# Kernel optimization log

Hardware: AMD Instinct MI355X
Metric: run time of the kernel (lower is better)

Reference implementation:

```python
import jax, jax.numpy as jnp
import numpy as np

B, C_IN, H, W = 4, 256, 56, 56
REL, OUT, SP, K, PAD = 16, 256, 8, 7, 3
WS = OUT // SP            # 32 attention-weight channels
K2 = K * K                # 49 window taps
EPS = 1e-5


def _unfold(x, k, pad):
    # reflect-pad (SAN pad_mode=1 -> *_refpad kernels) then gather kxk window taps
    # x: [B,C,H,W] -> [B,C,k*k,H,W], tap order row-major (matches torch Unfold)
    xp = jnp.pad(x, ((0, 0), (0, 0), (pad, pad), (pad, pad)), mode='reflect')
    h, w = x.shape[2], x.shape[3]
    return jnp.stack([xp[:, :, i:i + h, j:j + w]
                      for i in range(k) for j in range(k)], axis=2)


def _conv1x1(x, w, b):
    return jnp.einsum('bchw,oc->bohw', x, w) + b[None, :, None, None]


def _bn(x, g, b, m, v):
    # eval-mode BatchNorm2d over channel axis 1, broadcast over trailing dims
    shape = (1, -1) + (1,) * (x.ndim - 2)
    scale = g.reshape(shape) * jax.lax.rsqrt(v.reshape(shape) + EPS)
    return (x - m.reshape(shape)) * scale + b.reshape(shape)


def _forward(x, w1, b1, w2, b2, w3, b3,
             bn1_g, bn1_b, bn1_m, bn1_v, cw1_w,
             bn2_g, bn2_b, bn2_m, bn2_v, cw2_w, cw2_b, pos2_w):
    x1 = _conv1x1(x, w1, b1)          # [B,REL,H,W]  (query)
    x2 = _conv1x1(x, w2, b2)          # [B,REL,H,W]  (key)
    x3 = _conv1x1(x, w3, b3)          # [B,OUT,H,W]  (value)

    # Subtraction2: q_i - k_j for each of K2 window taps -> [B,REL,K2,H,W]
    diff = x1[:, :, None, :, :] - _unfold(x2, K, PAAD) if False else x1[:, :, None, :, :] - _unfold(x2, K, PAD)

    # conv_w: BN -> ReLU -> 1x1 (no bias) -> BN -> ReLU -> 1x1 (bias)
    h = jax.nn.relu(_bn(diff, bn1_g, bn1_b, bn1_m, bn1_v))
    h = jnp.einsum('bckhw,oc->bokhw', h, cw1_w)
    h = jax.nn.relu(_bn(h, bn2_g, bn2_b, bn2_m, bn2_v))
    h = jnp.einsum('bckhw,oc->bokhw', h, cw2_w) + cw2_b[None, :, None, None, None]
    w = jax.nn.softmax(h, axis=2)     # softmax over K2 taps -> [B,WS,K2,H,W]

    # Aggregation: out[b,c,p] = sum_k unfold(x3)[b,c,k,p] * w[b, c//SP, k, p]
    unf3 = _unfold(x3, K, PAD).reshape(B, WS, SP, K2, H, W)
    agg = jnp.einsum('bgskhw,bgkhw->bgshw', unf3, w).reshape(B, OUT, H, W)

    # use_position2: interleave aggregated values with w, grouped 1x1 conv
    xv = agg.reshape(B, SP, WS, H, W).transpose(0, 2, 1, 3, 4)   # [B,WS,SP,H,W]
    xc = jnp.concatenate([xv, w], axis=2)                        # [B,WS,SP+K2,H,W]
    out = jnp.einsum('bgihw,goi->bgohw', xc, pos2_w).reshape(B, OUT, H, W)
    return out


def setup_inputs() -> dict:
    key = jax.random.key(0)
    ks = jax.random.split(key, 20)
    n = lambda k, s, sc=1.0: jax.random.normal(k, s, dtype=jnp.float32) * sc
    u = lambda k, s: jax.random.uniform(k, s, dtype=jnp.float32, minval=0.5, maxval=1.5)
    return {
        'x': n(ks[0], (B, C_IN, H, W)),
        'w1': n(ks[1], (REL, C_IN), 0.05), 'b1': n(ks[2], (REL,), 0.05),
        'w2': n(ks[3], (REL, C_IN), 0.05), 'b2': n(ks[4], (REL,), 0.05),
        'w3': n(ks[5], (OUT, C_IN), 0.05), 'b3': n(ks[6], (OUT,), 0.05),
        'bn1_g': u(ks[7], (REL,)), 'bn1_b': n(ks[8], (REL,), 0.1),
        'bn1_m': n(ks[9], (REL,), 0.1), 'bn1_v': u(ks[10], (REL,)),
        'cw1_w': n(ks[11], (REL, REL), 0.2),
        'bn2_g': u(ks[12], (REL,)), 'bn2_b': n(ks[13], (REL,), 0.1),
        'bn2_m': n(ks[14], (REL,), 0.1), 'bn2_v': u(ks[15], (REL,)),
        'cw2_w': n(ks[16], (WS, REL), 0.2), 'cw2_b': n(ks[17], (WS,), 0.05),
        'pos2_w': n(ks[18], (WS, SP, SP + K2), 0.1),
    }


def reference(x, w1, b1, w2, b2, w3, b3,
              bn1_g, bn1_b, bn1_m, bn1_v, cw1_w,
              bn2_g, bn2_b, bn2_m, bn2_v, cw2_w, cw2_b, pos2_w):
    return _forward(x, w1, b1, w2, b2, w3, b3,
                    bn1_g, bn1_b, bn1_m, bn1_v, cw1_w,
                    bn2_g, bn2_b, bn2_m, bn2_v, cw2_w, cw2_b, pos2_w)
```

## Files before the change

kernel.cpp:

```cpp
#include <hip/hip_runtime.h>

#define HW 56
#define NPIX 3136
#define CIN 256
#define OUTC 256

typedef unsigned short ushort_t;
typedef unsigned int uint_t;
typedef __attribute__((ext_vector_type(8))) short bf16x8;
typedef __attribute__((ext_vector_type(4))) float f32x4;
typedef __attribute__((ext_vector_type(2))) __fp16 half2v;
typedef __attribute__((ext_vector_type(4))) _Float16 f16x4;

__device__ __forceinline__ ushort_t f2b(float f){
  uint_t u = __float_as_uint(f);
  u += 0x7fffu + ((u>>16)&1u);
  return (ushort_t)(u>>16);
}
__device__ __forceinline__ uint_t pkh2(float a, float b){
  union { half2v h; uint_t u; } pk;
  pk.h = __builtin_amdgcn_cvt_pkrtz(a, b);
  return pk.u;
}
__device__ __forceinline__ float h2lo(uint_t u){
  union { ushort_t s; __fp16 h; } c; c.s = (ushort_t)(u & 0xffffu); return (float)c.h;
}
__device__ __forceinline__ float h2hi(uint_t u){
  union { ushort_t s; __fp16 h; } c; c.s = (ushort_t)(u >> 16); return (float)c.h;
}
__device__ __forceinline__ int refl(int v){ v = v<0 ? -v : v; return v>=HW ? 2*HW-2-v : v; }

#define BF_OFF   40960
#define CW1B_OFF 41280
#define CW2B_OFF2 41536
#define CW2B_OFF 42048
#define BNC_OFF  42112
#define P2T_OFF  42176
#define P2H_OFF  56768
#define X1T_OFF  82368
#define X2T_OFF  283072
#define X3_BYTE_OFF 1935104

__global__ void k0_prep(const float* __restrict__ w1, const float* __restrict__ b1,
                        const float* __restrict__ w2, const float* __restrict__ b2,
                        const float* __restrict__ w3, const float* __restrict__ b3,
                        const float* __restrict__ g1, const float* __restrict__ be1,
                        const float* __restrict__ m1, const float* __restrict__ v1,
                        const float* __restrict__ cw1,
                        const float* __restrict__ g2, const float* __restrict__ be2,
                        const float* __restrict__ m2, const float* __restrict__ v2,
                        const float* __restrict__ cw2, const float* __restrict__ cw2b,
                        const float* __restrict__ p2,
                        float* __restrict__ ws)
{
  int idx = blockIdx.x*256 + threadIdx.x;
  if (idx < 81920){
    int j = idx & 7, l = (idx>>3)&63, t2 = idx>>9;
    int nf = t2 % 20, kt = t2 / 20;
    int k = kt*32 + (l>>4)*8 + j;
    int n = nf*16 + (l&15);
    float v = 0.f;
    if (n < 16)       v = w1[n*256 + k];
    else if (n < 32)  v = w2[(n-16)*256 + k];
    else if (n < 288) v = w3[(n-32)*256 + k];
    ((ushort_t*)ws)[idx] = f2b(v);
    return;
  }
  int j = idx - 81920;
  if (j < 288){ ws[BF_OFF+j] = (j<16 ? b1[j] : (j<32 ? b2[j-16] : b3[j-32])); return; }
  j -= 288;
  if (j < 32){ ws[BF_OFF+288+j] = 0.f; return; }
  j -= 32;
  if (j < 128){
    int l = j>>1, q = j&1;
    int n = l & 15, k = ((l>>4)<<2) + 2*q;
    union { __fp16 h[2]; uint_t u; } cv;
    cv.h[0] = (__fp16)cw1[n*16 + k];
    cv.h[1] = (__fp16)cw1[n*16 + k+1];
    ((uint_t*)ws)[CW1B_OFF + j] = cv.u;
    return;
  }
  j -= 128;
  if (j < 256){
    int nf = j>>7, rem = j&127, l = rem>>1, q = rem&1;
    int n = nf*16 + (l & 15), k = ((l>>4)<<2) + 2*q;
    union { __fp16 h[2]; uint_t u; } cv;
    cv.h[0] = (__fp16)cw2[n*16 + k];
    cv.h[1] = (__fp16)cw2[n*16 + k+1];
    ((uint_t*)ws)[CW2B_OFF2 + j] = cv.u;
    return;
  }
  j -= 256;
  if (j < 32){ ws[CW2B_OFF+j] = cw2b[j]; return; }
  j -= 32;
  if (j < 64){
    int set = j >> 4, c = j & 15;
    float o;
    if (set == 0){ o = g1[c] * rsqrtf(v1[c] + 1e-5f); }
    else if (set == 1){ float s = g1[c] * rsqrtf(v1[c] + 1e-5f); o = be1[c] - m1[c]*s; }
    else if (set == 2){ o = g2[c] * rsqrtf(v2[c] + 1e-5f); }
    else { float s = g2[c] * rsqrtf(v2[c] + 1e-5f); o = be2[c] - m2[c]*s; }
    ws[BNC_OFF+j] = o;
    return;
  }
  j -= 64;
  if (j < 14592){
    int i = j >> 8, rem = j & 255;
    ws[P2T_OFF + j] = p2[rem*57 + i];
    return;
  }
  j -= 14592;
  if (j < 25600){
    int p = j >> 8, c = j & 255;
    union { __fp16 h[2]; uint_t u; } cv;
    cv.h[0] = (__fp16)p2[c*57 + 8 + 2*p];
    cv.h[1] = (2*p+1 < 49) ? (__fp16)p2[c*57 + 9 + 2*p] : (__fp16)0.f;
    ((uint_t*)ws)[P2H_OFF + j] = cv.u;
    return;
  }
}

__global__ __launch_bounds__(256,2) void k1_proj(const float* __restrict__ x,
                                                 float* __restrict__ ws,
                                                 _Float16* __restrict__ x3h)
{
  __shared__ float xs[CIN*64];
  int t = threadIdx.x;
  int bid = blockIdx.x;
  int b = bid / 49, pp = (bid - b*49)*64;
  int wv = __builtin_amdgcn_readfirstlane(t >> 6);
  int lane = t & 63;

  {
    const float* src = x + (size_t)b*CIN*NPIX + pp;
    int c0 = t >> 4;
    int po = (t & 15) * 4;
    #pragma unroll
    for (int i=0;i<16;i++){
      const float* gp = src + (size_t)(i*16 + c0)*NPIX + po;
      __builtin_amdgcn_global_load_lds(
          (const __attribute__((address_space(1))) void*)gp,
          (__attribute__((address_space(3))) void*)(xs + i*1024 + wv*256),
          16, 0, 0);
    }
  }
  __syncthreads();

  f32x4 acc[4][5];
  float bias[5];
  #pragma unroll
  for (int nf=0;nf<5;nf++) bias[nf] = ws[BF_OFF + wv*80 + nf*16 + (lane&15)];
  #pragma unroll
  for (int m=0;m<4;m++)
    #pragma unroll
    for (int nf=0;nf<5;nf++)
      acc[m][nf] = (f32x4){bias[nf],bias[nf],bias[nf],bias[nf]};

  const uint4* bpk = (const uint4*)ws;
  #pragma unroll 1
  for (int kt=0;kt<8;kt++){
    int abase = (kt*32 + ((lane>>4)<<3))*64 + (lane&15);
    union { uint_t u[4]; bf16x8 v; } ahi[4], alo[4];
    #pragma unroll
    for (int m=0;m<4;m++){
      float f[8];
      #pragma unroll
      for (int j=0;j<8;j++) f[j] = xs[abase + j*64 + m*16];
      #pragma unroll
      for (int p=0;p<4;p++){
        uint_t u0 = __float_as_uint(f[2*p]), u1 = __float_as_uint(f[2*p+1]);
        uint_t h1 = u1 & 0xffff0000u;
        ahi[m].u[p] = (u0>>16) | h1;
        float l0 = f[2*p]   - __uint_as_float(u0 & 0xffff0000u);
        float l1 = f[2*p+1] - __uint_as_float(h1);
        alo[m].u[p] = (__float_as_uint(l0)>>16) | (__float_as_uint(l1) & 0xffff0000u);
      }
    }
    #pragma unroll
    for (int nf=0;nf<5;nf++){
      union { uint4 q; bf16x8 v; } bw;
      bw.q = bpk[(size_t)(kt*20 + wv*5 + nf)*64 + lane];
      #pragma unroll
      for (int m=0;m<4;m++){
        acc[m][nf] = __builtin_amdgcn_mfma_f32_16x16x32_bf16(ahi[m].v, bw.v, acc[m][nf], 0,0,0);
        acc[m][nf] = __builtin_amdgcn_mfma_f32_16x16x32_bf16(alo[m].v, bw.v, acc[m][nf], 0,0,0);
      }
    }
  }

  #pragma unroll
  for (int m=0;m<4;m++){
    #pragma unroll
    for (int r=0;r<4;r++){
      int sp = pp + m*16 + ((lane>>4)<<2) + r;
      #pragma unroll
      for (int nf=0;nf<5;nf++){
        int n = wv*80 + nf*16 + (lane&15);
        float val = acc[m][nf][r];
        if (n < 16){
          ws[X1T_OFF + (size_t)(b*NPIX + sp)*16 + n] = val;
        } else if (n < 32){
          ws[X2T_OFF + (size_t)(b*NPIX + sp)*16 + (n-16)] = val;
        } else if (n < 288){
          x3h[((size_t)b*NPIX + sp)*256 + (n-32)] = (_Float16)val;
        }
      }
    }
  }
}

__global__ __launch_bounds__(256,5) void k2_fused(const float* __restrict__ ws,
                                                  const _Float16* __restrict__ x3h,
                                                  float* __restrict__ out)
{
  __shared__ uint_t lgw[4*864];
  __shared__ ushort_t sA[4*1280];
  __shared__ int    gp_s[4*64];
  __shared__ __align__(16) float ags[4*256];

  int tid = threadIdx.x;
  int bid0 = blockIdx.x;
  int bid = (bid0 & 7)*392 + (bid0 >> 3);
  int b = bid / 784; int rem = bid - b*784;
  int row = rem / 14, xs4 = rem - row*14;
  int wv = __builtin_amdgcn_readfirstlane(tid >> 6);
  int lane = tid & 63;
  int y = row, x = xs4*4 + wv;
  int pix = y*HW + x;

  const float* bnc  = ws + BNC_OFF;
  const float* cw2b = ws + CW2B_OFF;
  uint_t* wvbase = lgw + wv*864;
  ushort_t* sAw = sA + wv*1280;
  int lrow = lane & 15, lk4 = (lane>>4)<<2;

  {
    int k = lane;
    int kk = k < 49 ? k : 48;
    int ki = kk / 7, kj = kk - ki*7;
    int gy = refl(y + ki - 3), gx = refl(x + kj - 3);
    int go = gy*HW + gx;
    gp_s[wv*64 + lane] = go << 9;

    const float*  x1p = ws + X1T_OFF + (size_t)(b*NPIX + pix)*16;
    const float4* x2p = (const float4*)(ws + X2T_OFF + (size_t)(b*NPIX + go)*16);
    float4 v0 = x2p[0], v1 = x2p[1], v2 = x2p[2], v3 = x2p[3];
    float x2v[16] = {v0.x,v0.y,v0.z,v0.w, v1.x,v1.y,v1.z,v1.w,
                     v2.x,v2.y,v2.z,v2.w, v3.x,v3.y,v3.z,v3.w};
    float h1[16];
    #pragma unroll
    for (int c=0;c<16;c++){
      float d = x1p[c] - x2v[c];
      h1[c] = fmaxf(d*bnc[c] + bnc[16+c], 0.f);
    }
    {
      uint2* dst = (uint2*)(sAw + lane*20);
      dst[0] = make_uint2(pkh2(h1[0],h1[1]),  pkh2(h1[2],h1[3]));
      dst[1] = make_uint2(pkh2(h1[4],h1[5]),  pkh2(h1[6],h1[7]));
      dst[2] = make_uint2(pkh2(h1[8],h1[9]),  pkh2(h1[10],h1[11]));
      dst[3] = make_uint2(pkh2(h1[12],h1[13]),pkh2(h1[14],h1[15]));
    }
    union { uint2 u; f16x4 h; } B1, B20, B21;
    B1.u  = ((const uint2*)((const uint_t*)ws + CW1B_OFF))[lane];
    B20.u = ((const uint2*)((const uint_t*)ws + CW2B_OFF2))[lane];
    B21.u = ((const uint2*)((const uint_t*)ws + CW2B_OFF2))[64 + lane];

    float bs2 = bnc[32+lrow], bb2 = bnc[48+lrow];
    #pragma unroll
    for (int m=0;m<4;m++){
      union { uint2 u; f16x4 h; } A;
      A.u = *(const uint2*)(sAw + (m*16+lrow)*20 + lk4);
      f32x4 d = __builtin_amdgcn_mfma_f32_16x16x16f16(A.h, B1.h, (f32x4){0.f,0.f,0.f,0.f}, 0,0,0);
      #pragma unroll
      for (int r=0;r<4;r++){
        float tv = fmaxf(d[r]*bs2 + bb2, 0.f);
        union { __fp16 h; ushort_t s; } th; th.h = (__fp16)tv;
        sAw[(m*16 + lk4 + r)*20 + lrow] = th.s;
      }
    }
    float bg0 = cw2b[lrow], bg1 = cw2b[16+lrow];
    #pragma unroll
    for (int m=0;m<4;m++){
      union { uint2 u; f16x4 h; } A2;
      A2.u = *(const uint2*)(sAw + (m*16+lrow)*20 + lk4);
      f32x4 d0 = __builtin_amdgcn_mfma_f32_16x16x16f16(A2.h, B20.h, (f32x4){bg0,bg0,bg0,bg0}, 0,0,0);
      f32x4 d1 = __builtin_amdgcn_mfma_f32_16x16x16f16(A2.h, B21.h, (f32x4){bg1,bg1,bg1,bg1}, 0,0,0);
      int pq = m*8 + ((lane>>4)<<1);
      uint_t p01 = pkh2(d0[0], d0[1]), p23 = pkh2(d0[2], d0[3]);
      uint_t q01 = pkh2(d1[0], d1[1]), q23 = pkh2(d1[2], d1[3]);
      if (pq < 25){
        wvbase[lrow*27 + pq]      = p01;
        wvbase[(16+lrow)*27 + pq] = q01;
      }
      if (pq+1 < 25){
        wvbase[lrow*27 + pq+1]      = p23;
        wvbase[(16+lrow)*27 + pq+1] = q23;
      }
    }
  }

  {
    int half = lane >> 5, g = lane & 31;
    const uint_t* lgp = wvbase + g*27;
    float e[25];
    float M = -3.0e38f;
    if (half == 0){
      #pragma unroll
      for (int j=0;j<12;j++){
        uint_t u = lgp[j];
        e[2*j]   = h2lo(u);
        e[2*j+1] = h2hi(u);
      }
      e[24] = h2lo(lgp[12]);
      #pragma unroll
      for (int i=0;i<25;i++) M = fmaxf(M, e[i]);
    } else {
      e[0] = h2hi(lgp[12]);
      #pragma unroll
      for (int j=0;j<11;j++){
        uint_t u = lgp[13+j];
        e[1+2*j] = h2lo(u);
        e[2+2*j] = h2hi(u);
      }
      e[23] = h2lo(lgp[24]);
      e[24] = 0.f;
      #pragma unroll
      for (int i=0;i<24;i++) M = fmaxf(M, e[i]);
    }
    M = fmaxf(M, __shfl_xor(M, 32, 64));
    float s = 0.f;
    #pragma unroll
    for (int i=0;i<25;i++){
      if (half == 0 || i < 24){
        e[i] = __expf(e[i] - M);
        s += e[i];
      }
    }
    s += __shfl_xor(s, 32, 64);
    float inv = 1.f / s;
    #pragma unroll
    for (int i=0;i<25;i++){
      if (half == 0 || i < 24) e[i] *= inv;
    }
    float other = __shfl_xor(half ? e[0] : e[24], 32, 64);
    if (half == 0){
      #pragma unroll
      for (int p=0;p<12;p++) wvbase[p*33 + g] = pkh2(e[2*p], e[2*p+1]);
      wvbase[12*33 + g] = pkh2(e[24], other);
    } else {
      #pragma unroll
      for (int q=0;q<11;q++) wvbase[(13+q)*33 + g] = pkh2(e[1+2*q], e[2+2*q]);
      wvbase[24*33 + g] = pkh2(e[23], 0.f);
    }
  }

  {
    int g_ = lane >> 1;
    int c0 = lane * 4;
    const int* gpp = gp_s + wv*64;
    float a0=0.f,a1=0.f,a2=0.f,a3=0.f;
    const char* xbb = (const char*)(x3h + (size_t)b*NPIX*256) + c0*2;
    #pragma unroll 5
    for (int p=0;p<25;p++){
      uint_t wu = wvbase[p*33 + g_];
      float w0 = h2lo(wu), w1 = h2hi(wu);
      int o0 = gpp[2*p], o1 = gpp[2*p+1];
      union { uint2 u; _Float16 h[4]; } d0, d1;
      d0.u = *(const uint2*)(xbb + o0);
      d1.u = *(const uint2*)(xbb + o1);
      a0 += w0*(float)d0.h[0] + w1*(float)d1.h[0];
      a1 += w0*(float)d0.h[1] + w1*(float)d1.h[1];
      a2 += w0*(float)d0.h[2] + w1*(float)d1.h[2];
      a3 += w0*(float)d0.h[3] + w1*(float)d1.h[3];
    }
    *(float4*)&ags[wv*256 + c0] = make_float4(a0,a1,a2,a3);
  }
  __syncthreads();

  {
    int c = tid, g4 = c >> 3;
    const float* P2 = ws + P2T_OFF;
    const uint_t* P2H = (const uint_t*)ws + P2H_OFF;
    float r0=0.f, r1=0.f, r2=0.f, r3=0.f;
    #pragma unroll
    for (int i=0;i<8;i++){
      float pv = P2[i*256 + c];
      r0 += ags[0*256 + i*32 + g4] * pv;
      r1 += ags[1*256 + i*32 + g4] * pv;
      r2 += ags[2*256 + i*32 + g4] * pv;
      r3 += ags[3*256 + i*32 + g4] * pv;
    }
    #pragma unroll 5
    for (int p=0;p<25;p++){
      union { uint_t u; half2v h; } ph; ph.u = P2H[p*256 + c];
      union { uint_t u; half2v h; } w0, w1, w2, w3;
      w0.u = lgw[0*864 + p*33 + g4];
      w1.u = lgw[1*864 + p*33 + g4];
      w2.u = lgw[2*864 + p*33 + g4];
      w3.u = lgw[3*864 + p*33 + g4];
      r0 = __builtin_amdgcn_fdot2(w0.h, ph.h, r0, false);
      r1 = __builtin_amdgcn_fdot2(w1.h, ph.h, r1, false);
      r2 = __builtin_amdgcn_fdot2(w2.h, ph.h, r2, false);
      r3 = __builtin_amdgcn_fdot2(w3.h, ph.h, r3, false);
    }
    int pix0 = y*HW + xs4*4;
    *(float4*)(out + ((size_t)(b*256 + c))*NPIX + pix0) = make_float4(r0,r1,r2,r3);
  }
}

extern "C" void kernel_launch(void* const* d_in, const int* in_sizes, int n_in,
                              void* d_out, int out_size, void* d_ws, size_t ws_size,
                              hipStream_t stream) {
  const float* x    = (const float*)d_in[0];
  const float* w1   = (const float*)d_in[1];
  const float* b1   = (const float*)d_in[2];
  const float* w2   = (const float*)d_in[3];
  const float* b2   = (const float*)d_in[4];
  const float* w3   = (const float*)d_in[5];
  const float* b3   = (const float*)d_in[6];
  const float* g1   = (const float*)d_in[7];
  const float* be1  = (const float*)d_in[8];
  const float* m1   = (const float*)d_in[9];
  const float* v1   = (const float*)d_in[10];
  const float* cw1  = (const float*)d_in[11];
  const float* g2   = (const float*)d_in[12];
  const float* be2  = (const float*)d_in[13];
  const float* m2   = (const float*)d_in[14];
  const float* v2   = (const float*)d_in[15];
  const float* cw2  = (const float*)d_in[16];
  const float* cw2b = (const float*)d_in[17];
  const float* p2   = (const float*)d_in[18];

  float* wsf = (float*)d_ws;
  _Float16* x3h = (_Float16*)((char*)d_ws + X3_BYTE_OFF);
  float* o = (float*)d_out;

  k0_prep<<<481, 256, 0, stream>>>(w1,b1,w2,b2,w3,b3,g1,be1,m1,v1,cw1,g2,be2,m2,v2,cw2,cw2b,p2,wsf);
  k1_proj<<<196, 256, 0, stream>>>(x, wsf, x3h);
  k2_fused<<<3136, 256, 0, stream>>>(wsf, x3h, o);
}
```

Before: 57.87 us.

## Shrink projection tiles, reuse LDS for aggregation, fold log2e into softmax weights

The projection kernel now processes 16 pixels per block instead of 64, launching four times as many blocks with less LDS and fewer accumulators, which lets it run at higher occupancy. The fused kernel drops its separate aggregation LDS buffer and reuses the sA scratch space, and raises the occupancy hint from 5 to 6. The softmax now uses exp2f, with log2e pre-multiplied into the second conv weights and bias during prep. The cost is reloading the projection weights across more blocks and a tighter register budget in the fused kernel.

```diff
diff --git a/kernel.cpp b/kernel.cpp
--- a/kernel.cpp
+++ b/kernel.cpp
@@ -4,6 +4,7 @@
 #define NPIX 3136
 #define CIN 256
 #define OUTC 256
+#define LOG2E 1.4426950408889634f
 
 typedef unsigned short ushort_t;
 typedef unsigned int uint_t;
@@ -85,13 +86,13 @@
     int nf = j>>7, rem = j&127, l = rem>>1, q = rem&1;
     int n = nf*16 + (l & 15), k = ((l>>4)<<2) + 2*q;
     union { __fp16 h[2]; uint_t u; } cv;
-    cv.h[0] = (__fp16)cw2[n*16 + k];
-    cv.h[1] = (__fp16)cw2[n*16 + k+1];
+    cv.h[0] = (__fp16)(cw2[n*16 + k]   * LOG2E);
+    cv.h[1] = (__fp16)(cw2[n*16 + k+1] * LOG2E);
     ((uint_t*)ws)[CW2B_OFF2 + j] = cv.u;
     return;
   }
   j -= 256;
-  if (j < 32){ ws[CW2B_OFF+j] = cw2b[j]; return; }
+  if (j < 32){ ws[CW2B_OFF+j] = cw2b[j] * LOG2E; return; }
   j -= 32;
   if (j < 64){
     int set = j >> 4, c = j & 15;
@@ -120,24 +121,24 @@
   }
 }
 
-__global__ __launch_bounds__(256,2) void k1_proj(const float* __restrict__ x,
+__global__ __launch_bounds__(256,4) void k1_proj(const float* __restrict__ x,
                                                  float* __restrict__ ws,
                                                  _Float16* __restrict__ x3h)
 {
-  __shared__ float xs[CIN*64];
+  __shared__ float xs[CIN*16];
   int t = threadIdx.x;
   int bid = blockIdx.x;
-  int b = bid / 49, pp = (bid - b*49)*64;
+  int b = bid / 196, pp = (bid - b*196)*16;
   int wv = __builtin_amdgcn_readfirstlane(t >> 6);
   int lane = t & 63;
 
   {
     const float* src = x + (size_t)b*CIN*NPIX + pp;
-    int c0 = t >> 4;
-    int po = (t & 15) * 4;
-    #pragma unroll
-    for (int i=0;i<16;i++){
-      const float* gp = src + (size_t)(i*16 + c0)*NPIX + po;
+    int c0 = t >> 2;
+    int po = (t & 3) * 4;
+    #pragma unroll
+    for (int i=0;i<4;i++){
+      const float* gp = src + (size_t)(i*64 + c0)*NPIX + po;
       __builtin_amdgcn_global_load_lds(
           (const __attribute__((address_space(1))) void*)gp,
           (__attribute__((address_space(3))) void*)(xs + i*1024 + wv*256),
@@ -146,77 +147,66 @@
   }
   __syncthreads();
 
-  f32x4 acc[4][5];
-  float bias[5];
+  f32x4 acc[5];
   #pragma unroll
-  for (int nf=0;nf<5;nf++) bias[nf] = ws[BF_OFF + wv*80 + nf*16 + (lane&15)];
-  #pragma unroll
-  for (int m=0;m<4;m++)
-    #pragma unroll
-    for (int nf=0;nf<5;nf++)
-      acc[m][nf] = (f32x4){bias[nf],bias[nf],bias[nf],bias[nf]};
+  for (int nf=0;nf<5;nf++){
+    float bv = ws[BF_OFF + wv*80 + nf*16 + (lane&15)];
+    acc[nf] = (f32x4){bv,bv,bv,bv};
+  }
 
   const uint4* bpk = (const uint4*)ws;
   #pragma unroll 1
   for (int kt=0;kt<8;kt++){
-    int abase = (kt*32 + ((lane>>4)<<3))*64 + (lane&15);
-    union { uint_t u[4]; bf16x8 v; } ahi[4], alo[4];
-    #pragma unroll
-    for (int m=0;m<4;m++){
+    int abase = (kt*32 + ((lane>>4)<<3))*16 + (lane&15);
+    union { uint_t u[4]; bf16x8 v; } ahi, alo;
+    {
       float f[8];
       #pragma unroll
-      for (int j=0;j<8;j++) f[j] = xs[abase + j*64 + m*16];
+      for (int j=0;j<8;j++) f[j] = xs[abase + j*16];
       #pragma unroll
       for (int p=0;p<4;p++){
         uint_t u0 = __float_as_uint(f[2*p]), u1 = __float_as_uint(f[2*p+1]);
         uint_t h1 = u1 & 0xffff0000u;
-        ahi[m].u[p] = (u0>>16) | h1;
+        ahi.u[p] = (u0>>16) | h1;
         float l0 = f[2*p]   - __uint_as_float(u0 & 0xffff0000u);
         float l1 = f[2*p+1] - __uint_as_float(h1);
-        alo[m].u[p] = (__float_as_uint(l0)>>16) | (__float_as_uint(l1) & 0xffff0000u);
+        alo.u[p] = (__float_as_uint(l0)>>16) | (__float_as_uint(l1) & 0xffff0000u);
       }
     }
     #pragma unroll
     for (int nf=0;nf<5;nf++){
       union { uint4 q; bf16x8 v; } bw;
       bw.q = bpk[(size_t)(kt*20 + wv*5 + nf)*64 + lane];
-      #pragma unroll
-      for (int m=0;m<4;m++){
-        acc[m][nf] = __builtin_amdgcn_mfma_f32_16x16x32_bf16(ahi[m].v, bw.v, acc[m][nf], 0,0,0);
-        acc[m][nf] = __builtin_amdgcn_mfma_f32_16x16x32_bf16(alo[m].v, bw.v, acc[m][nf], 0,0,0);
-      }
+      acc[nf] = __builtin_amdgcn_mfma_f32_16x16x32_bf16(ahi.v, bw.v, acc[nf], 0,0,0);
+      acc[nf] = __builtin_amdgcn_mfma_f32_16x16x32_bf16(alo.v, bw.v, acc[nf], 0,0,0);
     }
   }
 
   #pragma unroll
-  for (int m=0;m<4;m++){
-    #pragma unroll
-    for (int r=0;r<4;r++){
-      int sp = pp + m*16 + ((lane>>4)<<2) + r;
-      #pragma unroll
-      for (int nf=0;nf<5;nf++){
-        int n = wv*80 + nf*16 + (lane&15);
-        float val = acc[m][nf][r];
-        if (n < 16){
-          ws[X1T_OFF + (size_t)(b*NPIX + sp)*16 + n] = val;
-        } else if (n < 32){
-          ws[X2T_OFF + (size_t)(b*NPIX + sp)*16 + (n-16)] = val;
-        } else if (n < 288){
-          x3h[((size_t)b*NPIX + sp)*256 + (n-32)] = (_Float16)val;
-        }
-      }
-    }
-  }
-}
-
-__global__ __launch_bounds__(256,5) void k2_fused(const float* __restrict__ ws,
+  for (int r=0;r<4;r++){
+    int sp = pp + ((lane>>4)<<2) + r;
+    #pragma unroll
+    for (int nf=0;nf<5;nf++){
+      int n = wv*80 + nf*16 + (lane&15);
+      float val = acc[nf][r];
+      if (n < 16){
+        ws[X1T_OFF + (size_t)(b*NPIX + sp)*16 + n] = val;
+      } else if (n < 32){
+        ws[X2T_OFF + (size_t)(b*NPIX + sp)*16 + (n-16)] = val;
+      } else if (n < 288){
+        x3h[((size_t)b*NPIX + sp)*256 + (n-32)] = (_Float16)val;
+      }
+    }
+  }
+}
+
+__global__ __launch_bounds__(256,6) void k2_fused(const float* __restrict__ ws,
                                                   const _Float16* __restrict__ x3h,
                                                   float* __restrict__ out)
 {
   __shared__ uint_t lgw[4*864];
-  __shared__ ushort_t sA[4*1280];
+  __shared__ __align__(16) ushort_t sA[4*1280];
   __shared__ int    gp_s[4*64];
-  __shared__ __align__(16) float ags[4*256];
 
   int tid = threadIdx.x;
   int bid0 = blockIdx.x;
@@ -332,7 +322,7 @@
     #pragma unroll
     for (int i=0;i<25;i++){
       if (half == 0 || i < 24){
-        e[i] = __expf(e[i] - M);
+        e[i] = exp2f(e[i] - M);
         s += e[i];
       }
     }
@@ -373,7 +363,8 @@
       a2 += w0*(float)d0.h[2] + w1*(float)d1.h[2];
       a3 += w0*(float)d0.h[3] + w1*(float)d1.h[3];
     }
-    *(float4*)&ags[wv*256 + c0] = make_float4(a0,a1,a2,a3);
+    float* agw = (float*)(sA + wv*1280);
+    *(float4*)&agw[c0] = make_float4(a0,a1,a2,a3);
   }
   __syncthreads();
 
@@ -381,14 +372,18 @@
     int c = tid, g4 = c >> 3;
     const float* P2 = ws + P2T_OFF;
     const uint_t* P2H = (const uint_t*)ws + P2H_OFF;
+    const float* ag0 = (const float*)(sA + 0*1280);
+    const float* ag1 = (const float*)(sA + 1*1280);
+    const float* ag2 = (const float*)(sA + 2*1280);
+    const float* ag3 = (const float*)(sA + 3*1280);
     float r0=0.f, r1=0.f, r2=0.f, r3=0.f;
     #pragma unroll
     for (int i=0;i<8;i++){
       float pv = P2[i*256 + c];
-      r0 += ags[0*256 + i*32 + g4] * pv;
-      r1 += ags[1*256 + i*32 + g4] * pv;
-      r2 += ags[2*256 + i*32 + g4] * pv;
-      r3 += ags[3*256 + i*32 + g4] * pv;
+      r0 += ag0[i*32 + g4] * pv;
+      r1 += ag1[i*32 + g4] * pv;
+      r2 += ag2[i*32 + g4] * pv;
+      r3 += ag3[i*32 + g4] * pv;
     }
     #pragma unroll 5
     for (int p=0;p<25;p++){
@@ -436,6 +431,6 @@
   float* o = (float*)d_out;
 
   k0_prep<<<481, 256, 0, stream>>>(w1,b1,w2,b2,w3,b3,g1,be1,m1,v1,cw1,g2,be2,m2,v2,cw2,cw2b,p2,wsf);
-  k1_proj<<<196, 256, 0, stream>>>(x, wsf, x3h);
+  k1_proj<<<784, 256, 0, stream>>>(x, wsf, x3h);
   k2_fused<<<3136, 256, 0, stream>>>(wsf, x3h, o);
 }
```

Result: no change. 57.56 us (-0.5%).
